# Kernel optimization log

Measured on AMD Instinct MI355X. Metric: run time of the kernel, lower is better.

## Reference

```python
import jax, jax.numpy as jnp
import numpy as np

B, D = 8192, 768
TOP_K = 5


def setup_inputs() -> dict:
    key = jax.random.key(0)
    ks = jax.random.split(key, 12)
    # xavier_uniform bound for (D, D)
    bg = float(np.sqrt(6.0 / (D + D)))
    def xav(k, fan_in, fan_out):
        b = float(np.sqrt(6.0 / (fan_in + fan_out)))
        return jax.random.uniform(k, (fan_in, fan_out), jnp.float32, -b, b)
    return {
        "X": jax.random.normal(ks[0], (B, D), jnp.float32),
        "A_ecfp": jax.random.uniform(ks[1], (B, B), jnp.float32),
        "W_g": jax.random.uniform(ks[2], (D, D), jnp.float32, -bg, bg),
        "raw_alpha": jnp.zeros((), jnp.float32),
        "W_gcn": xav(ks[3], D, D),
        "b_gcn": jnp.zeros((D,), jnp.float32),
        "W1": xav(ks[4], D, 512),
        "b1": jnp.zeros((512,), jnp.float32),
        "W2": xav(ks[5], 512, 256),
        "b2": jnp.zeros((256,), jnp.float32),
        "W3": xav(ks[6], 256, 1),
        "b3": jnp.zeros((1,), jnp.float32),
    }


def _forward(X, A_ecfp, W_g, raw_alpha, W_gcn, b_gcn, W1, b1, W2, b2, W3, b3):
    n = X.shape[0]
    # learned similarity, blended with ECFP prior
    S = jax.nn.relu((X @ W_g) @ X.T)                    # (B, B)
    alpha = jax.nn.sigmoid(raw_alpha)
    A = alpha * A_ecfp + (1.0 - alpha) * S
    # top-k sparsification per row, symmetrized (OR)
    k = min(TOP_K, n - 1)
    _, top_idx = jax.lax.top_k(A, k)                    # (B, k)
    rows = jnp.arange(n)[:, None]
    mask = jnp.zeros_like(A).at[rows, top_idx].set(1.0)
    mask = ((mask + mask.T) > 0).astype(A.dtype)
    A = A * mask
    # zero diagonal, then add self-loops (diagonal becomes 1)
    diag = jnp.eye(n, dtype=A.dtype)
    A = A * (1.0 - diag) + diag
    # degree normalization D^-1 A
    D_inv = 1.0 / jnp.clip(A.sum(-1, keepdims=True), 1e-8)
    A_norm = A * D_inv
    # single GCN layer (exact erf GELU, matching torch default)
    H = jax.nn.gelu(A_norm @ X @ W_gcn + b_gcn, approximate=False)
    # MLP head (dropout is identity in eval)
    h = jax.nn.gelu(H @ W1 + b1, approximate=False)
    h = jax.nn.gelu(h @ W2 + b2, approximate=False)
    return h @ W3 + b3                                  # (B, 1)


def reference(X, A_ecfp, W_g, raw_alpha, W_gcn, b_gcn, W1, b1, W2, b2, W3, b3):
    return _forward(X, A_ecfp, W_g, raw_alpha, W_gcn, b_gcn, W1, b1, W2, b2, W3, b3)
```

## Files before the change

kernel.cpp:

```cpp
#include <hip/hip_runtime.h>
#include <math.h>


typedef __attribute__((ext_vector_type(8))) short short8v;
typedef __attribute__((ext_vector_type(4))) float f32x4;

__device__ __forceinline__ unsigned short f2bf(float f) {
  unsigned u = __float_as_uint(f);
  u += 0x7fffu + ((u >> 16) & 1u);
  return (unsigned short)(u >> 16);
}
__device__ __forceinline__ float bf2f(unsigned short h) {
  return __uint_as_float(((unsigned)h) << 16);
}
__device__ __forceinline__ float gelu_f(float x) {
  return 0.5f * x * (1.f + erff(x * 0.7071067811865475f));
}
__device__ __forceinline__ void gload16(const void* g, void* l) {
  __builtin_amdgcn_global_load_lds(
      (const __attribute__((address_space(1))) unsigned int*)g,
      (__attribute__((address_space(3))) unsigned int*)l, 16, 0, 0);
}

template <int N>
__device__ __forceinline__ void insN(float v, int j, float (&lv)[N], int (&li)[N]) {
#pragma unroll
  for (int p = N - 1; p >= 1; --p) {
    bool shiftv = v > lv[p - 1];
    bool here = (v > lv[p]) && !shiftv;
    float nv = shiftv ? lv[p - 1] : (here ? v : lv[p]);
    int ni = shiftv ? li[p - 1] : (here ? j : li[p]);
    lv[p] = nv; li[p] = ni;
  }
  if (v > lv[0]) { lv[0] = v; li[0] = j; }
}

__global__ __launch_bounds__(256) void cvt_bf16(const float* __restrict__ in,
                                                unsigned short* __restrict__ out, int n4) {
  int t = blockIdx.x * 256 + threadIdx.x;
  if (t >= n4) return;
  float4 f = ((const float4*)in)[t];
  ushort4 r;
  r.x = f2bf(f.x); r.y = f2bf(f.y); r.z = f2bf(f.z); r.w = f2bf(f.w);
  ((ushort4*)out)[t] = r;
}

__global__ __launch_bounds__(256) void split2(const float* __restrict__ in,
                                              unsigned short* __restrict__ out,
                                              int K, int n4) {
  int t = blockIdx.x * 256 + threadIdx.x;
  if (t >= n4) return;
  int kq = K >> 2;
  int row = t / kq, c4 = t - row * kq;
  float4 f = ((const float4*)in)[t];
  ushort4 h, l;
  float x;
  x = f.x; h.x = f2bf(x); l.x = f2bf(x - bf2f(h.x));
  x = f.y; h.y = f2bf(x); l.y = f2bf(x - bf2f(h.y));
  x = f.z; h.z = f2bf(x); l.z = f2bf(x - bf2f(h.z));
  x = f.w; h.w = f2bf(x); l.w = f2bf(x - bf2f(h.w));
  *(ushort4*)(out + (size_t)row * 2 * K + c4 * 4) = h;
  *(ushort4*)(out + (size_t)row * 2 * K + K + c4 * 4) = l;
}

__global__ __launch_bounds__(256) void split_wt2(const float* __restrict__ W,
                                                 unsigned short* __restrict__ t2,
                                                 int K, int N) {
  __shared__ float tile[32][33];
  int kb = blockIdx.x * 32, nb = blockIdx.y * 32;
  int tx = threadIdx.x & 31, ty = threadIdx.x >> 5;
#pragma unroll
  for (int p = 0; p < 4; ++p)
    tile[ty + p * 8][tx] = W[(size_t)(kb + ty + p * 8) * N + nb + tx];
  __syncthreads();
#pragma unroll
  for (int p = 0; p < 4; ++p) {
    int n = ty + p * 8;
    float x = tile[tx][n];
    unsigned short h = f2bf(x);
    unsigned short l = f2bf(x - bf2f(h));
    t2[(size_t)(nb + n) * (2 * K) + kb + tx] = h;
    t2[(size_t)(nb + n) * (2 * K) + K + kb + tx] = l;
  }
}

__global__ __launch_bounds__(256) void sgemm_f32(const float* __restrict__ A,
                                                 const float* __restrict__ Bm,
                                                 float* __restrict__ C, int N, int K) {
  __shared__ float As[16][68];
  __shared__ float Bs[16][132];
  const int r0 = blockIdx.x * 64, c0 = blockIdx.y * 128;
  const int tid = threadIdx.x;
  const int tr = tid >> 4, tc = tid & 15;
  float acc[4][8];
#pragma unroll
  for (int i = 0; i < 4; ++i)
#pragma unroll
    for (int j = 0; j < 8; ++j) acc[i][j] = 0.f;

  for (int k0 = 0; k0 < K; k0 += 16) {
    {
      int row = tid >> 2, kq = tid & 3;
      float4 a4 = *(const float4*)(A + (size_t)(r0 + row) * K + k0 + kq * 4);
      As[kq * 4 + 0][row] = a4.x; As[kq * 4 + 1][row] = a4.y;
      As[kq * 4 + 2][row] = a4.z; As[kq * 4 + 3][row] = a4.w;
#pragma unroll
      for (int s = 0; s < 2; ++s) {
        int ch = tid + s * 256;
        int kk = ch >> 5, nq = ch & 31;
        *(float4*)&Bs[kk][nq * 4] = *(const float4*)(Bm + (size_t)(k0 + kk) * N + c0 + nq * 4);
      }
    }
    __syncthreads();
#pragma unroll
    for (int k = 0; k < 16; ++k) {
      float a[4], b[8];
      *(float4*)&a[0] = *(const float4*)&As[k][tr * 4];
      *(float4*)&b[0] = *(const float4*)&Bs[k][tc * 8];
      *(float4*)&b[4] = *(const float4*)&Bs[k][tc * 8 + 4];
#pragma unroll
      for (int i = 0; i < 4; ++i)
#pragma unroll
        for (int j = 0; j < 8; ++j) acc[i][j] = fmaf(a[i], b[j], acc[i][j]);
    }
    __syncthreads();
  }
#pragma unroll
  for (int i = 0; i < 4; ++i) {
    int r = r0 + tr * 4 + i;
#pragma unroll
    for (int jq = 0; jq < 2; ++jq)
      *(float4*)(C + (size_t)r * N + c0 + tc * 8 + jq * 4) = *(float4*)&acc[i][jq * 4];
  }
}

template <int EPI>
__global__ __launch_bounds__(256) void gemm_bt(const unsigned short* __restrict__ A,
                                               const unsigned short* __restrict__ Bt,
                                               const float* __restrict__ bias,
                                               float* __restrict__ C, int N, int K) {
  __shared__ __align__(16) unsigned short As[128 * 64];
  __shared__ __align__(16) unsigned short Bs[128 * 64];
  const int r0 = blockIdx.x * 128, c0 = blockIdx.y * 128;
  const int tid = threadIdx.x, lane = tid & 63, w = tid >> 6;
  const int wr = w >> 1, wc = w & 1;
  f32x4 acc[4][4];
  const f32x4 z4 = {0.f, 0.f, 0.f, 0.f};
#pragma unroll
  for (int i = 0; i < 4; ++i)
#pragma unroll
    for (int j = 0; j < 4; ++j) acc[i][j] = z4;

  const int srow = w * 32 + (lane >> 3);
  const int ksl = (lane & 7) ^ (lane >> 3);
  const unsigned short* aSrc = A + (size_t)(r0 + srow) * K + ksl * 8;
  const unsigned short* bSrc = Bt + (size_t)(c0 + srow) * K + ksl * 8;
  const int rsw = (lane & 7);

  for (int k0 = 0; k0 < K; k0 += 64) {
#pragma unroll
    for (int t = 0; t < 4; ++t) {
      gload16(aSrc + k0 + (size_t)t * 8 * K, (char*)As + (w * 32 + t * 8) * 128);
      gload16(bSrc + k0 + (size_t)t * 8 * K, (char*)Bs + (w * 32 + t * 8) * 128);
    }
    __syncthreads();
#pragma unroll
    for (int ks = 0; ks < 2; ++ks) {
      short8v af[4], bf[4];
      const int slot = ((ks * 4 + (lane >> 4)) ^ rsw) << 4;
#pragma unroll
      for (int f = 0; f < 4; ++f) {
        af[f] = *(const short8v*)((const char*)As + (wr * 64 + f * 16 + (lane & 15)) * 128 + slot);
        bf[f] = *(const short8v*)((const char*)Bs + (wc * 64 + f * 16 + (lane & 15)) * 128 + slot);
      }
#pragma unroll
      for (int fi = 0; fi < 4; ++fi)
#pragma unroll
        for (int fj = 0; fj < 4; ++fj)
          acc[fi][fj] = __builtin_amdgcn_mfma_f32_16x16x32_bf16(af[fi], bf[fj], acc[fi][fj], 0, 0, 0);
    }
    __syncthreads();
  }
#pragma unroll
  for (int fi = 0; fi < 4; ++fi)
#pragma unroll
    for (int fj = 0; fj < 4; ++fj) {
      int col = c0 + wc * 64 + fj * 16 + (lane & 15);
      int rowb = r0 + wr * 64 + fi * 16 + (lane >> 4) * 4;
#pragma unroll
      for (int r = 0; r < 4; ++r) {
        size_t idx = (size_t)(rowb + r) * N + col;
        float x = acc[fi][fj][r];
        if constexpr (EPI) x = gelu_f(x + bias[col]);
        C[idx] = x;
      }
    }
}

__global__ __launch_bounds__(512, 4) void s_topk(const unsigned short* __restrict__ Gh,
                                                 const unsigned short* __restrict__ Xh,
                                                 float* __restrict__ pv, int* __restrict__ pix) {
  __shared__ __align__(16) unsigned short As[128 * 64];
  __shared__ __align__(16) unsigned short Bs[128 * 64];
  __shared__ __align__(16) unsigned short St[128 * 128];
  const int r0 = blockIdx.x * 128;
  const int chunk = blockIdx.y;
  const int tid = threadIdx.x, lane = tid & 63, w = tid >> 6;
  const int wr = w >> 2, wc = w & 3;
  float lv[8]; int li[8];
#pragma unroll
  for (int q = 0; q < 8; ++q) { lv[q] = -1e30f; li[q] = 0; }

  const int strow = tid >> 3, sslot = tid & 7;
  const int ksl = sslot ^ (strow & 7);
  const unsigned short* aSrc = Gh + (size_t)(r0 + strow) * 768 + ksl * 8;
  char* aDst0 = (char*)As + strow * 128 + sslot * 16;
  char* bDst0 = (char*)Bs + strow * 128 + sslot * 16;
  const int rsw = (lane & 7);
  const int srow = tid & 127, sg = tid >> 7;

  for (int jt = 0; jt < 8; ++jt) {
    const int j0 = chunk * 1024 + jt * 128;
    const unsigned short* bSrc = Xh + (size_t)(j0 + strow) * 768 + ksl * 8;
    f32x4 acc[4][2];
    const f32x4 z4 = {0.f, 0.f, 0.f, 0.f};
#pragma unroll
    for (int i = 0; i < 4; ++i)
#pragma unroll
      for (int j = 0; j < 2; ++j) acc[i][j] = z4;

    for (int k0 = 0; k0 < 768; k0 += 64) {
      gload16(aSrc + k0, aDst0);
      gload16(aSrc + k0 + (size_t)64 * 768, aDst0 + 64 * 128);
      gload16(bSrc + k0, bDst0);
      gload16(bSrc + k0 + (size_t)64 * 768, bDst0 + 64 * 128);
      __syncthreads();
#pragma unroll
      for (int ks = 0; ks < 2; ++ks) {
        short8v af[4], bf[2];
        const int slot = ((ks * 4 + (lane >> 4)) ^ rsw) << 4;
#pragma unroll
        for (int f = 0; f < 4; ++f)
          af[f] = *(const short8v*)((const char*)As + (wr * 64 + f * 16 + (lane & 15)) * 128 + slot);
#pragma unroll
        for (int f = 0; f < 2; ++f)
          bf[f] = *(const short8v*)((const char*)Bs + (wc * 32 + f * 16 + (lane & 15)) * 128 + slot);
#pragma unroll
        for (int fi = 0; fi < 4; ++fi)
#pragma unroll
          for (int fj = 0; fj < 2; ++fj)
            acc[fi][fj] = __builtin_amdgcn_mfma_f32_16x16x32_bf16(af[fi], bf[fj], acc[fi][fj], 0, 0, 0);
      }
      __syncthreads();
    }
#pragma unroll
    for (int fi = 0; fi < 4; ++fi)
#pragma unroll
      for (int fj = 0; fj < 2; ++fj) {
        int col = wc * 32 + fj * 16 + (lane & 15);
#pragma unroll
        for (int r = 0; r < 4; ++r) {
          int row = wr * 64 + fi * 16 + (lane >> 4) * 4 + r;
          int byo = (row * 256 + col * 2) ^ ((row & 7) << 4);
          *(unsigned short*)((char*)St + byo) = f2bf(acc[fi][fj][r]);
        }
      }
    __syncthreads();
#pragma unroll
    for (int cb = 0; cb < 4; ++cb) {
      int byo = (srow * 256 + sg * 64 + cb * 16) ^ ((srow & 7) << 4);
      short8v v8 = *(const short8v*)((const char*)St + byo);
#pragma unroll
      for (int e = 0; e < 8; ++e) {
        float v = bf2f((unsigned short)v8[e]);
        if (v > lv[7]) insN<8>(v, j0 + sg * 32 + cb * 8 + e, lv, li);
      }
    }
    __syncthreads();
  }
  size_t basep = (((size_t)(r0 + srow) * 8 + chunk) * 4 + sg) * 8;
#pragma unroll
  for (int q = 0; q < 8; ++q) { pv[basep + q] = lv[q]; pix[basep + q] = li[q]; }
}

__global__ __launch_bounds__(256) void merge16(const float* __restrict__ pv,
                                               const int* __restrict__ pix,
                                               int* __restrict__ gidx) {
  int row = blockIdx.x * 256 + threadIdx.x;
  float lv[16]; int li[16];
#pragma unroll
  for (int q = 0; q < 16; ++q) { lv[q] = -1e30f; li[q] = 0; }
  for (int ch = 0; ch < 8; ++ch)
#pragma unroll
    for (int g = 0; g < 4; ++g) {
      size_t base = (((size_t)row * 8 + ch) * 4 + g) * 8;
#pragma unroll
      for (int q = 0; q < 8; ++q) {
        float v = pv[base + q];
        if (v > lv[15]) insN<16>(v, pix[base + q], lv, li);
      }
    }
#pragma unroll
  for (int q = 0; q < 16; ++q) gidx[row * 16 + q] = li[q];
}

__global__ __launch_bounds__(256) void refine5(const float* __restrict__ G,
                                               const float* __restrict__ X,
                                               const float* __restrict__ Ae,
                                               const int* __restrict__ gidx,
                                               const float* __restrict__ ralpha,
                                               int* __restrict__ t5i, float* __restrict__ t5v) {
  int i = blockIdx.x * 4 + (threadIdx.x >> 6);
  int lane = threadIdx.x & 63;
  int c = lane >> 2, s = lane & 3;
  float sa = 1.f / (1.f + expf(-ralpha[0]));
  int j = gidx[i * 16 + c];
  const float* g = G + (size_t)i * 768;
  const float* x = X + (size_t)j * 768;
  float a = 0.f;
#pragma unroll 8
  for (int t = 0; t < 192; ++t) a = fmaf(g[s + 4 * t], x[s + 4 * t], a);
  a += __shfl_xor(a, 1);
  a += __shfl_xor(a, 2);
  float v = sa * Ae[(size_t)i * 8192 + j] + (1.f - sa) * fmaxf(a, 0.f);
  float vs[16]; int js[16];
#pragma unroll
  for (int q = 0; q < 16; ++q) { vs[q] = __shfl(v, q * 4); js[q] = __shfl(j, q * 4); }
  if (lane == 0) {
    unsigned used = 0;
#pragma unroll
    for (int t = 0; t < 5; ++t) {
      float bv = -1e30f; int bj = 0; int bq = 0; bool any = false;
#pragma unroll
      for (int q = 0; q < 16; ++q) {
        bool ok = ((used >> q) & 1u) == 0u;
        bool better = ok && (!any || vs[q] > bv || (vs[q] == bv && js[q] < bj));
        bv = better ? vs[q] : bv; bj = better ? js[q] : bj; bq = better ? q : bq;
        any = any || better;
      }
      used |= (1u << bq);
      t5v[(size_t)i * 5 + t] = bv;
      t5i[(size_t)i * 5 + t] = bj;
    }
  }
}

__global__ void edge_deg(const int* __restrict__ t5i, int* __restrict__ deg) {
  int e = blockIdx.x * 256 + threadIdx.x;
  if (e >= 40960) return;
  int i = e / 5, t = e - i * 5;
  int j = t5i[i * 5 + t];
  if (j == i) return;
  bool rev = false;
#pragma unroll
  for (int u = 0; u < 5; ++u) rev = rev || (t5i[j * 5 + u] == i);
  if (!rev || i < j) { atomicAdd(&deg[i], 1); atomicAdd(&deg[j], 1); }
}

__global__ void scan8k(const int* __restrict__ deg, int* __restrict__ off) {
  __shared__ int sums[256];
  int tid = threadIdx.x;
  int base = tid * 32;
  int s = 0;
  for (int u = 0; u < 32; ++u) s += deg[base + u];
  sums[tid] = s;
  __syncthreads();
  for (int d = 1; d < 256; d <<= 1) {
    int v = (tid >= d) ? sums[tid - d] : 0;
    __syncthreads();
    sums[tid] += v;
    __syncthreads();
  }
  int run = tid ? sums[tid - 1] : 0;
  for (int u = 0; u < 32; ++u) { off[base + u] = run; run += deg[base + u]; }
  if (tid == 255) off[8192] = run;
}

__global__ __launch_bounds__(256) void edge_fill(const int* __restrict__ t5i,
                                                 const float* __restrict__ t5v,
                                                 const float* __restrict__ G,
                                                 const float* __restrict__ X,
                                                 const float* __restrict__ Ae,
                                                 const float* __restrict__ ralpha,
                                                 const int* __restrict__ off,
                                                 int* __restrict__ cursor,
                                                 int* __restrict__ ccol, float* __restrict__ cval) {
  int e = blockIdx.x * 4 + (threadIdx.x >> 6);
  if (e >= 40960) return;
  int lane = threadIdx.x & 63;
  int i = e / 5, t = e - i * 5;
  int j = t5i[i * 5 + t];
  if (j == i) return;
  int rev = -1;
#pragma unroll
  for (int u = 0; u < 5; ++u)
    if (t5i[j * 5 + u] == i) rev = u;
  if (!(rev < 0 || i < j)) return;
  float vji;
  if (rev >= 0) {
    vji = t5v[j * 5 + rev];
  } else {
    const float* g = G + (size_t)j * 768;
    const float* x = X + (size_t)i * 768;
    float a = 0.f;
#pragma unroll
    for (int u = 0; u < 12; ++u) a = fmaf(g[lane + 64 * u], x[lane + 64 * u], a);
#pragma unroll
    for (int d = 32; d; d >>= 1) a += __shfl_xor(a, d);
    float sa = 1.f / (1.f + expf(-ralpha[0]));
    vji = sa * Ae[(size_t)j * 8192 + i] + (1.f - sa) * fmaxf(a, 0.f);
  }
  if (lane == 0) {
    float vij = t5v[i * 5 + t];
    int p0 = off[i] + atomicAdd(&cursor[i], 1);
    ccol[p0] = j; cval[p0] = vij;
    int p1 = off[j] + atomicAdd(&cursor[j], 1);
    ccol[p1] = i; cval[p1] = vji;
  }
}

__global__ __launch_bounds__(256) void gather_gcn(const float* __restrict__ X,
                                                  const int* __restrict__ off,
                                                  const int* __restrict__ ccol,
                                                  const float* __restrict__ cval,
                                                  float* __restrict__ M) {
  __shared__ float red[256];
  __shared__ float sdinv;
  int i = blockIdx.x, tid = threadIdx.x;
  int s0 = off[i], cnt = off[i + 1] - s0;
  float s = 0.f;
  for (int e = tid; e < cnt; e += 256) s += cval[s0 + e];
  red[tid] = s;
  __syncthreads();
  for (int d = 128; d; d >>= 1) {
    if (tid < d) red[tid] += red[tid + d];
    __syncthreads();
  }
  if (tid == 0) sdinv = 1.f / fmaxf(1.f + red[0], 1e-8f);
  __syncthreads();
  float dinv = sdinv;
  const float* xi = X + (size_t)i * 768;
  float a0 = xi[tid], a1 = xi[tid + 256], a2 = xi[tid + 512];
  for (int e = 0; e < cnt; ++e) {
    float v = cval[s0 + e];
    const float* xr = X + (size_t)ccol[s0 + e] * 768;
    a0 = fmaf(v, xr[tid], a0);
    a1 = fmaf(v, xr[tid + 256], a1);
    a2 = fmaf(v, xr[tid + 512], a2);
  }
  float* mi = M + (size_t)i * 768;
  mi[tid] = a0 * dinv; mi[tid + 256] = a1 * dinv; mi[tid + 512] = a2 * dinv;
}

__global__ __launch_bounds__(256) void final_head(const float* __restrict__ h2,
                                                  const float* __restrict__ W3,
                                                  const float* __restrict__ b3,
                                                  float* __restrict__ out) {
  int i = blockIdx.x * 4 + (threadIdx.x >> 6);
  int lane = threadIdx.x & 63;
  const float* r = h2 + (size_t)i * 256;
  float s = r[lane] * W3[lane] + r[lane + 64] * W3[lane + 64] +
            r[lane + 128] * W3[lane + 128] + r[lane + 192] * W3[lane + 192];
#pragma unroll
  for (int d = 32; d; d >>= 1) s += __shfl_xor(s, d);
  if (lane == 0) out[i] = s + b3[0];
}

extern "C" void kernel_launch(void* const* d_in, const int* in_sizes, int n_in,
                              void* d_out, int out_size, void* d_ws, size_t ws_size,
                              hipStream_t stream) {
  const float* X   = (const float*)d_in[0];
  const float* Ae  = (const float*)d_in[1];
  const float* Wg  = (const float*)d_in[2];
  const float* ra  = (const float*)d_in[3];
  const float* Wgc = (const float*)d_in[4];
  const float* bgc = (const float*)d_in[5];
  const float* W1  = (const float*)d_in[6];
  const float* b1  = (const float*)d_in[7];
  const float* W2  = (const float*)d_in[8];
  const float* b2  = (const float*)d_in[9];
  const float* W3  = (const float*)d_in[10];
  const float* b3  = (const float*)d_in[11];
  float* out = (float*)d_out;

  char* w = (char*)d_ws;
  size_t off_ = 0;
  auto take = [&](size_t n) -> void* {
    void* p = w + off_;
    off_ += (n + 255) & ~(size_t)255;
    return p;
  };
  float* G            = (float*)take((size_t)8192 * 768 * 4);
  unsigned short* Xh  = (unsigned short*)take((size_t)8192 * 768 * 2);
  unsigned short* Gh  = (unsigned short*)take((size_t)8192 * 768 * 2);
  float* pv           = (float*)take((size_t)8192 * 256 * 4);
  int* pix            = (int*)take((size_t)8192 * 256 * 4);
  int* gidx           = (int*)take((size_t)8192 * 16 * 4);
  int* t5i            = (int*)take((size_t)8192 * 5 * 4);
  float* t5v          = (float*)take((size_t)8192 * 5 * 4);
  int* deg            = (int*)take((size_t)8192 * 4);
  int* offr           = (int*)take((size_t)8193 * 4);
  int* cur            = (int*)take((size_t)8192 * 4);
  int* ccol           = (int*)take((size_t)81920 * 4);
  float* cval         = (float*)take((size_t)81920 * 4);
  unsigned short* Wc2 = (unsigned short*)take((size_t)768 * 1536 * 2);
  unsigned short* W12 = (unsigned short*)take((size_t)512 * 1536 * 2);
  unsigned short* W22 = (unsigned short*)take((size_t)256 * 1024 * 2);

  float* Mf  = (float*)Xh;
  float* Hf  = (float*)Xh;
  float* h1f = (float*)Xh;
  unsigned short* A2 = (unsigned short*)G;
  float* h2f = (float*)pv;

  sgemm_f32<<<dim3(128, 6), 256, 0, stream>>>(X, Wg, G, 768, 768);
  cvt_bf16<<<6144, 256, 0, stream>>>(X, Xh, 1572864);
  cvt_bf16<<<6144, 256, 0, stream>>>(G, Gh, 1572864);
  split_wt2<<<dim3(24, 24), 256, 0, stream>>>(Wgc, Wc2, 768, 768);
  split_wt2<<<dim3(24, 16), 256, 0, stream>>>(W1, W12, 768, 512);
  split_wt2<<<dim3(16, 8), 256, 0, stream>>>(W2, W22, 512, 256);

  s_topk<<<dim3(64, 8), 512, 0, stream>>>(Gh, Xh, pv, pix);
  merge16<<<32, 256, 0, stream>>>(pv, pix, gidx);
  refine5<<<2048, 256, 0, stream>>>(G, X, Ae, gidx, ra, t5i, t5v);

  hipMemsetAsync(deg, 0, 8192 * 4, stream);
  hipMemsetAsync(cur, 0, 8192 * 4, stream);
  edge_deg<<<160, 256, 0, stream>>>(t5i, deg);
  scan8k<<<1, 256, 0, stream>>>(deg, offr);
  edge_fill<<<10240, 256, 0, stream>>>(t5i, t5v, G, X, Ae, ra, offr, cur, ccol, cval);

  gather_gcn<<<8192, 256, 0, stream>>>(X, offr, ccol, cval, Mf);

  split2<<<6144, 256, 0, stream>>>(Mf, A2, 768, 1572864);
  gemm_bt<1><<<dim3(64, 6), 256, 0, stream>>>(A2, Wc2, bgc, Hf, 768, 1536);

  split2<<<6144, 256, 0, stream>>>(Hf, A2, 768, 1572864);
  gemm_bt<1><<<dim3(64, 4), 256, 0, stream>>>(A2, W12, b1, h1f, 512, 1536);

  split2<<<4096, 256, 0, stream>>>(h1f, A2, 512, 1048576);
  gemm_bt<1><<<dim3(64, 2), 256, 0, stream>>>(A2, W22, b2, h2f, 256, 1024);

  final_head<<<2048, 256, 0, stream>>>(h2f, W3, b3, out);

  (void)in_sizes; (void)n_in; (void)out_size; (void)ws_size;
}
```

Measured before the change: 721.7 us.

## Fuse bf16 conversion into sgemm and run top-k directly on MFMA registers

The sgemm now writes a bf16 copy of G alongside the fp32 result, which removes a separate conversion kernel. The s_topk kernel swaps operand roles so each lane's MFMA accumulator holds candidates for fixed rows. It keeps per-lane top-5 lists in registers, dropping the LDS staging tile and its extra barriers. The partial-candidate layout grows from 32×8 to 64×5 per row chunk and merge16 is adapted to read it, which adds merge work and workspace. Taking only top-5 per lane slot could change which candidates survive compared with the previous top-8 per group.

```diff
diff --git a/kernel.cpp b/kernel.cpp
--- a/kernel.cpp
+++ b/kernel.cpp
@@ -86,7 +86,9 @@
 
 __global__ __launch_bounds__(256) void sgemm_f32(const float* __restrict__ A,
                                                  const float* __restrict__ Bm,
-                                                 float* __restrict__ C, int N, int K) {
+                                                 float* __restrict__ C,
+                                                 unsigned short* __restrict__ Cbf,
+                                                 int N, int K) {
   __shared__ float As[16][68];
   __shared__ float Bs[16][132];
   const int r0 = blockIdx.x * 64, c0 = blockIdx.y * 128;
@@ -129,8 +131,13 @@
   for (int i = 0; i < 4; ++i) {
     int r = r0 + tr * 4 + i;
 #pragma unroll
-    for (int jq = 0; jq < 2; ++jq)
+    for (int jq = 0; jq < 2; ++jq) {
       *(float4*)(C + (size_t)r * N + c0 + tc * 8 + jq * 4) = *(float4*)&acc[i][jq * 4];
+      ushort4 hb;
+      hb.x = f2bf(acc[i][jq * 4 + 0]); hb.y = f2bf(acc[i][jq * 4 + 1]);
+      hb.z = f2bf(acc[i][jq * 4 + 2]); hb.w = f2bf(acc[i][jq * 4 + 3]);
+      *(ushort4*)(Cbf + (size_t)r * N + c0 + tc * 8 + jq * 4) = hb;
+    }
   }
 }
 
@@ -202,32 +209,33 @@
                                                  float* __restrict__ pv, int* __restrict__ pix) {
   __shared__ __align__(16) unsigned short As[128 * 64];
   __shared__ __align__(16) unsigned short Bs[128 * 64];
-  __shared__ __align__(16) unsigned short St[128 * 128];
-  const int r0 = blockIdx.x * 128;
-  const int chunk = blockIdx.y;
+  const int bid = blockIdx.x;
+  const int r0 = (bid >> 3) * 128;
+  const int chunk = bid & 7;
   const int tid = threadIdx.x, lane = tid & 63, w = tid >> 6;
   const int wr = w >> 2, wc = w & 3;
-  float lv[8]; int li[8];
-#pragma unroll
-  for (int q = 0; q < 8; ++q) { lv[q] = -1e30f; li[q] = 0; }
+  float lv0[5], lv1[5]; int li0[5], li1[5];
+#pragma unroll
+  for (int q = 0; q < 5; ++q) {
+    lv0[q] = -1e30f; li0[q] = 0; lv1[q] = -1e30f; li1[q] = 0;
+  }
 
   const int strow = tid >> 3, sslot = tid & 7;
   const int ksl = sslot ^ (strow & 7);
-  const unsigned short* aSrc = Gh + (size_t)(r0 + strow) * 768 + ksl * 8;
+  const unsigned short* bSrc = Gh + (size_t)(r0 + strow) * 768 + ksl * 8;
   char* aDst0 = (char*)As + strow * 128 + sslot * 16;
   char* bDst0 = (char*)Bs + strow * 128 + sslot * 16;
-  const int rsw = (lane & 7);
-  const int srow = tid & 127, sg = tid >> 7;
+  const int rsw = lane & 7;
 
   for (int jt = 0; jt < 8; ++jt) {
     const int j0 = chunk * 1024 + jt * 128;
-    const unsigned short* bSrc = Xh + (size_t)(j0 + strow) * 768 + ksl * 8;
+    const unsigned short* aSrc = Xh + (size_t)(j0 + strow) * 768 + ksl * 8;
     f32x4 acc[4][2];
     const f32x4 z4 = {0.f, 0.f, 0.f, 0.f};
 #pragma unroll
-    for (int i = 0; i < 4; ++i)
-#pragma unroll
-      for (int j = 0; j < 2; ++j) acc[i][j] = z4;
+    for (int i = 0; i < 4; ++i) {
+      acc[i][0] = z4; acc[i][1] = z4;
+    }
 
     for (int k0 = 0; k0 < 768; k0 += 64) {
       gload16(aSrc + k0, aDst0);
@@ -237,50 +245,42 @@
       __syncthreads();
 #pragma unroll
       for (int ks = 0; ks < 2; ++ks) {
-        short8v af[4], bf[2];
+        short8v aj[4], bi[2];
         const int slot = ((ks * 4 + (lane >> 4)) ^ rsw) << 4;
 #pragma unroll
         for (int f = 0; f < 4; ++f)
-          af[f] = *(const short8v*)((const char*)As + (wr * 64 + f * 16 + (lane & 15)) * 128 + slot);
+          aj[f] = *(const short8v*)((const char*)As + (wr * 64 + f * 16 + (lane & 15)) * 128 + slot);
 #pragma unroll
         for (int f = 0; f < 2; ++f)
-          bf[f] = *(const short8v*)((const char*)Bs + (wc * 32 + f * 16 + (lane & 15)) * 128 + slot);
-#pragma unroll
-        for (int fi = 0; fi < 4; ++fi)
-#pragma unroll
-          for (int fj = 0; fj < 2; ++fj)
-            acc[fi][fj] = __builtin_amdgcn_mfma_f32_16x16x32_bf16(af[fi], bf[fj], acc[fi][fj], 0, 0, 0);
+          bi[f] = *(const short8v*)((const char*)Bs + (wc * 32 + f * 16 + (lane & 15)) * 128 + slot);
+#pragma unroll
+        for (int fi = 0; fi < 4; ++fi) {
+          acc[fi][0] = __builtin_amdgcn_mfma_f32_16x16x32_bf16(aj[fi], bi[0], acc[fi][0], 0, 0, 0);
+          acc[fi][1] = __builtin_amdgcn_mfma_f32_16x16x32_bf16(aj[fi], bi[1], acc[fi][1], 0, 0, 0);
+        }
       }
       __syncthreads();
     }
+    const int jb = j0 + wr * 64 + (lane >> 4) * 4;
 #pragma unroll
     for (int fi = 0; fi < 4; ++fi)
 #pragma unroll
-      for (int fj = 0; fj < 2; ++fj) {
-        int col = wc * 32 + fj * 16 + (lane & 15);
-#pragma unroll
-        for (int r = 0; r < 4; ++r) {
-          int row = wr * 64 + fi * 16 + (lane >> 4) * 4 + r;
-          int byo = (row * 256 + col * 2) ^ ((row & 7) << 4);
-          *(unsigned short*)((char*)St + byo) = f2bf(acc[fi][fj][r]);
-        }
-      }
-    __syncthreads();
-#pragma unroll
-    for (int cb = 0; cb < 4; ++cb) {
-      int byo = (srow * 256 + sg * 64 + cb * 16) ^ ((srow & 7) << 4);
-      short8v v8 = *(const short8v*)((const char*)St + byo);
-#pragma unroll
-      for (int e = 0; e < 8; ++e) {
-        float v = bf2f((unsigned short)v8[e]);
-        if (v > lv[7]) insN<8>(v, j0 + sg * 32 + cb * 8 + e, lv, li);
-      }
-    }
-    __syncthreads();
-  }
-  size_t basep = (((size_t)(r0 + srow) * 8 + chunk) * 4 + sg) * 8;
-#pragma unroll
-  for (int q = 0; q < 8; ++q) { pv[basep + q] = lv[q]; pix[basep + q] = li[q]; }
+      for (int r = 0; r < 4; ++r) {
+        int jj = jb + fi * 16 + r;
+        float v0 = acc[fi][0][r];
+        if (v0 > lv0[4]) insN<5>(v0, jj, lv0, li0);
+        float v1 = acc[fi][1][r];
+        if (v1 > lv1[4]) insN<5>(v1, jj, lv1, li1);
+      }
+  }
+  const int slotw = wr * 4 + (lane >> 4);
+  const int ib0 = r0 + wc * 32 + (lane & 15);
+  size_t base0 = (((size_t)ib0 * 8 + chunk) * 8 + slotw) * 5;
+#pragma unroll
+  for (int q = 0; q < 5; ++q) { pv[base0 + q] = lv0[q]; pix[base0 + q] = li0[q]; }
+  size_t base1 = (((size_t)(ib0 + 16) * 8 + chunk) * 8 + slotw) * 5;
+#pragma unroll
+  for (int q = 0; q < 5; ++q) { pv[base1 + q] = lv1[q]; pix[base1 + q] = li1[q]; }
 }
 
 __global__ __launch_bounds__(256) void merge16(const float* __restrict__ pv,
@@ -292,10 +292,10 @@
   for (int q = 0; q < 16; ++q) { lv[q] = -1e30f; li[q] = 0; }
   for (int ch = 0; ch < 8; ++ch)
 #pragma unroll
-    for (int g = 0; g < 4; ++g) {
-      size_t base = (((size_t)row * 8 + ch) * 4 + g) * 8;
-#pragma unroll
-      for (int q = 0; q < 8; ++q) {
+    for (int sl = 0; sl < 8; ++sl) {
+      size_t base = (((size_t)row * 8 + ch) * 8 + sl) * 5;
+#pragma unroll
+      for (int q = 0; q < 5; ++q) {
         float v = pv[base + q];
         if (v > lv[15]) insN<16>(v, pix[base + q], lv, li);
       }
@@ -493,8 +493,8 @@
   float* G            = (float*)take((size_t)8192 * 768 * 4);
   unsigned short* Xh  = (unsigned short*)take((size_t)8192 * 768 * 2);
   unsigned short* Gh  = (unsigned short*)take((size_t)8192 * 768 * 2);
-  float* pv           = (float*)take((size_t)8192 * 256 * 4);
-  int* pix            = (int*)take((size_t)8192 * 256 * 4);
+  float* pv           = (float*)take((size_t)8192 * 320 * 4);
+  int* pix            = (int*)take((size_t)8192 * 320 * 4);
   int* gidx           = (int*)take((size_t)8192 * 16 * 4);
   int* t5i            = (int*)take((size_t)8192 * 5 * 4);
   float* t5v          = (float*)take((size_t)8192 * 5 * 4);
@@ -513,14 +513,13 @@
   unsigned short* A2 = (unsigned short*)G;
   float* h2f = (float*)pv;
 
-  sgemm_f32<<<dim3(128, 6), 256, 0, stream>>>(X, Wg, G, 768, 768);
+  sgemm_f32<<<dim3(128, 6), 256, 0, stream>>>(X, Wg, G, Gh, 768, 768);
   cvt_bf16<<<6144, 256, 0, stream>>>(X, Xh, 1572864);
-  cvt_bf16<<<6144, 256, 0, stream>>>(G, Gh, 1572864);
   split_wt2<<<dim3(24, 24), 256, 0, stream>>>(Wgc, Wc2, 768, 768);
   split_wt2<<<dim3(24, 16), 256, 0, stream>>>(W1, W12, 768, 512);
   split_wt2<<<dim3(16, 8), 256, 0, stream>>>(W2, W22, 512, 256);
 
-  s_topk<<<dim3(64, 8), 512, 0, stream>>>(Gh, Xh, pv, pix);
+  s_topk<<<512, 512, 0, stream>>>(Gh, Xh, pv, pix);
   merge16<<<32, 256, 0, stream>>>(pv, pix, gidx);
   refine5<<<2048, 256, 0, stream>>>(G, X, Ae, gidx, ra, t5i, t5v);
 
```

Result: no change. 717.8 us (-0.5%).
